# Optimization experiments

Hardware: AMD Instinct MI355X
Metric: run time of the kernel (lower is better)

The kernel has to match this reference:

```python
import jax, jax.numpy as jnp
import numpy as np

N_HEADS = 16
KQ_DIM = 64
EMB_DIM = 1024
CTX_DIM = 1024
EPS = 1e-5

def _layernorm(x, w, b):
    # LayerNorm over last dim (kq_dim), elementwise affine
    mu = jnp.mean(x, axis=-1, keepdims=True)
    var = jnp.mean(jnp.square(x - mu), axis=-1, keepdims=True)
    return (x - mu) * jax.lax.rsqrt(var + EPS) * w + b

def setup_inputs() -> dict:
    key = jax.random.key(0)
    ks = jax.random.split(key, 10)
    B, SQ, SK = 2, 2048, 2048
    inner = N_HEADS * KQ_DIM
    s_e = 1.0 / np.sqrt(EMB_DIM)
    s_c = 1.0 / np.sqrt(CTX_DIM)
    s_i = 1.0 / np.sqrt(inner)
    return {
        "emb": jax.random.normal(ks[0], (B, SQ, EMB_DIM), jnp.float32),
        "context": jax.random.normal(ks[1], (B, SK, CTX_DIM), jnp.float32),
        "Wq": jax.random.uniform(ks[2], (inner, EMB_DIM), jnp.float32, -s_e, s_e),
        "Wk": jax.random.uniform(ks[3], (inner, CTX_DIM), jnp.float32, -s_c, s_c),
        "Wv": jax.random.uniform(ks[4], (inner, CTX_DIM), jnp.float32, -s_c, s_c),
        "Wu": jax.random.uniform(ks[5], (EMB_DIM, inner), jnp.float32, -s_i, s_i),
        "bu": jax.random.uniform(ks[6], (EMB_DIM,), jnp.float32, -s_i, s_i),
        "qn_w": jnp.ones((KQ_DIM,), jnp.float32),
        "qn_b": jnp.zeros((KQ_DIM,), jnp.float32),
        "kn_w": jnp.ones((KQ_DIM,), jnp.float32),
        "kn_b": jnp.zeros((KQ_DIM,), jnp.float32),
    }

def reference(emb, context, Wq, Wk, Wv, Wu, bu, qn_w, qn_b, kn_w, kn_b):
    B, SQ, _ = emb.shape
    SK = context.shape[1]
    # projections (no bias), reshape to [B, H, S, D]
    q = (emb @ Wq.T).reshape(B, SQ, N_HEADS, KQ_DIM).transpose(0, 2, 1, 3)
    k = (context @ Wk.T).reshape(B, SK, N_HEADS, KQ_DIM).transpose(0, 2, 1, 3)
    v = (context @ Wv.T).reshape(B, SK, N_HEADS, KQ_DIM).transpose(0, 2, 1, 3)
    q = _layernorm(q, qn_w, qn_b)
    k = _layernorm(k, kn_w, kn_b)
    scale = 1.0 / jnp.sqrt(jnp.asarray(KQ_DIM, emb.dtype))
    attn = jnp.einsum('bhqd,bhkd->bhqk', q, k) * scale
    attn = jax.nn.softmax(attn, axis=-1)
    out = jnp.einsum('bhqk,bhkd->bhqd', attn, v)
    out = out.transpose(0, 2, 1, 3).reshape(B, SQ, N_HEADS * KQ_DIM)
    return out @ Wu.T + bu
```

## Files before the change

### kernel.cpp

```cpp
#include <hip/hip_runtime.h>


typedef __attribute__((ext_vector_type(8)))  short bf16x8;
typedef __attribute__((ext_vector_type(4)))  short bf16x4;
typedef __attribute__((ext_vector_type(4)))  float f32x4;
typedef __attribute__((ext_vector_type(16))) float f32x16;
typedef __attribute__((ext_vector_type(4)))  unsigned int u32x4;

typedef __attribute__((address_space(1))) const void cg_void;
typedef __attribute__((address_space(3))) void lds_void_t;

__device__ __forceinline__ void gl_lds16(const void* g, void* l){
  __builtin_amdgcn_global_load_lds((cg_void*)g, (lds_void_t*)l, 16, 0, 0);
}

__device__ __forceinline__ short f2b(float f){
  unsigned int u;
  __builtin_memcpy(&u, &f, 4);
  u += 0x7fffu + ((u >> 16) & 1u);
  return (short)(u >> 16);
}

__global__ __launch_bounds__(256) void cvt6_kernel(
    const float* __restrict__ emb, const float* __restrict__ ctx,
    const float* __restrict__ Wq, const float* __restrict__ Wk,
    const float* __restrict__ Wv, const float* __restrict__ Wu,
    short* __restrict__ o_emb, short* __restrict__ o_ctx,
    short* __restrict__ o_wq, short* __restrict__ o_wk,
    short* __restrict__ o_wv, short* __restrict__ o_wu)
{
  const long M1 = 1024L * 1024L, M4 = 4L * M1;
  long e = ((long)blockIdx.x * 256 + threadIdx.x) * 4;
  if (e >= 12L * M1) return;
  const float* src; short* dst; long off;
  if      (e <     M4)      { src = emb; dst = o_emb; off = e;           }
  else if (e < 2 * M4)      { src = ctx; dst = o_ctx; off = e - M4;      }
  else if (e < 2 * M4 + M1) { src = Wq;  dst = o_wq;  off = e - 2 * M4;  }
  else if (e < 2 * M4 + 2*M1){src = Wk;  dst = o_wk;  off = e - 2*M4 - M1;}
  else if (e < 2 * M4 + 3*M1){src = Wv;  dst = o_wv;  off = e - 2*M4 - 2*M1;}
  else                      { src = Wu;  dst = o_wu;  off = e - 2*M4 - 3*M1;}
  f32x4 v = *(const f32x4*)(src + off);
  bf16x4 o;
  o[0] = f2b(v[0]); o[1] = f2b(v[1]); o[2] = f2b(v[2]); o[3] = f2b(v[3]);
  *(bf16x4*)(dst + off) = o;
}

__global__ __launch_bounds__(256) void gemm_qkv_kernel(
    const short* __restrict__ embh, const short* __restrict__ ctxh,
    const short* __restrict__ Wqh, const short* __restrict__ Wkh,
    const short* __restrict__ Wvh,
    short* __restrict__ qo, short* __restrict__ ko, short* __restrict__ vto,
    const float* __restrict__ qw, const float* __restrict__ qb,
    const float* __restrict__ kw, const float* __restrict__ kb)
{
  const int K = 1024;
  __shared__ short As[128 * 64];
  __shared__ short Bs[128 * 64];
  const int tid  = threadIdx.x;
  const int wave = tid >> 6, lane = tid & 63;
  const int quad = lane >> 4, r16 = lane & 15;
  const int wm = (wave >> 1) * 64, wn = (wave & 1) * 64;

  const int task = blockIdx.y;
  int bn, bm, N;
  const short *A, *B;
  if (task == 2){
    bn = (blockIdx.x & 31) * 128; bm = (blockIdx.x >> 5) * 128; N = 4096;
    A = Wvh; B = ctxh;
  } else {
    bn = (blockIdx.x & 7) * 128; bm = (blockIdx.x >> 3) * 128; N = 1024;
    A = task ? ctxh : embh; B = task ? Wkh : Wqh;
  }

  f32x4 acc[4][4];
#pragma unroll
  for (int i = 0; i < 4; i++)
#pragma unroll
    for (int j = 0; j < 4; j++)
      acc[i][j] = (f32x4){0.f, 0.f, 0.f, 0.f};

  const size_t arow = (size_t)(bm + wave * 8 + (lane >> 3)) * K + (lane & 7) * 8;
  const size_t brow = (size_t)(bn + wave * 8 + (lane >> 3)) * K + (lane & 7) * 8;

  for (int k0 = 0; k0 < K; k0 += 64){
#pragma unroll
    for (int i = 0; i < 4; i++){
      gl_lds16(A + arow + (size_t)32 * i * K + k0, &As[wave * 512 + i * 2048]);
      gl_lds16(B + brow + (size_t)32 * i * K + k0, &Bs[wave * 512 + i * 2048]);
    }
    __syncthreads();
#pragma unroll
    for (int kk = 0; kk < 2; kk++){
      bf16x8 af[4], bq[4];
#pragma unroll
      for (int i = 0; i < 4; i++)
        af[i] = *(const bf16x8*)(&As[(wm + i*16 + r16) * 64 + kk*32 + quad*8]);
#pragma unroll
      for (int j = 0; j < 4; j++)
        bq[j] = *(const bf16x8*)(&Bs[(wn + j*16 + r16) * 64 + kk*32 + quad*8]);
#pragma unroll
      for (int i = 0; i < 4; i++)
#pragma unroll
        for (int j = 0; j < 4; j++)
          acc[i][j] = __builtin_amdgcn_mfma_f32_16x16x32_bf16(af[i], bq[j], acc[i][j], 0, 0, 0);
    }
    __syncthreads();
  }

  if (task < 2){
    short* Ch = task ? ko : qo;
    const float* lw = task ? kw : qw;
    const float* lb = task ? kb : qb;
    float wv[4], bv[4];
#pragma unroll
    for (int j = 0; j < 4; j++){ wv[j] = lw[j*16 + r16]; bv[j] = lb[j*16 + r16]; }
#pragma unroll
    for (int i = 0; i < 4; i++){
#pragma unroll
      for (int t = 0; t < 4; t++){
        float a[4];
#pragma unroll
        for (int j = 0; j < 4; j++) a[j] = acc[i][j][t];
        float s = a[0] + a[1] + a[2] + a[3];
        s += __shfl_xor(s, 1); s += __shfl_xor(s, 2);
        s += __shfl_xor(s, 4); s += __shfl_xor(s, 8);
        const float mu = s * 0.015625f;
        float d[4], sq = 0.f;
#pragma unroll
        for (int j = 0; j < 4; j++){ d[j] = a[j] - mu; sq += d[j]*d[j]; }
        sq += __shfl_xor(sq, 1); sq += __shfl_xor(sq, 2);
        sq += __shfl_xor(sq, 4); sq += __shfl_xor(sq, 8);
        const float si = rsqrtf(sq * 0.015625f + 1e-5f);
        const size_t row = (size_t)(bm + wm + i*16 + quad*4 + t);
#pragma unroll
        for (int j = 0; j < 4; j++)
          Ch[row * 1024 + (bn + wn + j*16 + r16)] = f2b(d[j] * si * wv[j] + bv[j]);
      }
    }
  } else {
#pragma unroll
    for (int i = 0; i < 4; i++){
#pragma unroll
      for (int j = 0; j < 4; j++){
        const int p = (r16 & 3) | ((j & 1) << 2) | (((r16 >> 2) & 1) << 3)
                      | (((r16 >> 3) & 1) << 4);
        const int col = ((bn + wn + j*16 + r16) & ~31) | p;
#pragma unroll
        for (int t = 0; t < 4; t++){
          const size_t row = (size_t)(bm + wm + i*16 + quad*4 + t);
          vto[row * (size_t)N + col] = f2b(acc[i][j][t]);
        }
      }
    }
  }
}

__global__ __launch_bounds__(256) void gemm_out_kernel(
    const short* __restrict__ A, const short* __restrict__ B,
    float* __restrict__ Cf, const float* __restrict__ bias)
{
  const int K = 1024, N = 1024;
  __shared__ short As[128 * 128];
  __shared__ short Bs[128 * 128];
  const int tid  = threadIdx.x;
  const int wave = tid >> 6, lane = tid & 63;
  const int quad = lane >> 4, r16 = lane & 15;
  const int wm = (wave >> 1) * 64, wn = (wave & 1) * 64;
  const int bm = blockIdx.y * 128, bn = blockIdx.x * 128;

  f32x4 acc[4][4];
#pragma unroll
  for (int i = 0; i < 4; i++)
#pragma unroll
    for (int j = 0; j < 4; j++)
      acc[i][j] = (f32x4){0.f, 0.f, 0.f, 0.f};

  const size_t arow = (size_t)(bm + wave * 4 + (lane >> 4)) * K + (lane & 15) * 8;
  const size_t brow = (size_t)(bn + wave * 4 + (lane >> 4)) * K + (lane & 15) * 8;

  for (int k0 = 0; k0 < K; k0 += 128){
#pragma unroll
    for (int i = 0; i < 8; i++){
      gl_lds16(A + arow + (size_t)16 * i * K + k0, &As[(wave * 4 + i * 16) * 128]);
      gl_lds16(B + brow + (size_t)16 * i * K + k0, &Bs[(wave * 4 + i * 16) * 128]);
    }
    __syncthreads();
#pragma unroll
    for (int kk = 0; kk < 4; kk++){
      bf16x8 af[4], bq[4];
#pragma unroll
      for (int i = 0; i < 4; i++)
        af[i] = *(const bf16x8*)(&As[(wm + i*16 + r16) * 128 + kk*32 + quad*8]);
#pragma unroll
      for (int j = 0; j < 4; j++)
        bq[j] = *(const bf16x8*)(&Bs[(wn + j*16 + r16) * 128 + kk*32 + quad*8]);
#pragma unroll
      for (int i = 0; i < 4; i++)
#pragma unroll
        for (int j = 0; j < 4; j++)
          acc[i][j] = __builtin_amdgcn_mfma_f32_16x16x32_bf16(af[i], bq[j], acc[i][j], 0, 0, 0);
    }
    __syncthreads();
  }

#pragma unroll
  for (int i = 0; i < 4; i++){
#pragma unroll
    for (int j = 0; j < 4; j++){
      const int col = bn + wn + j*16 + r16;
#pragma unroll
      for (int t = 0; t < 4; t++){
        const size_t row = (size_t)(bm + wm + i*16 + quad*4 + t);
        Cf[row * N + col] = acc[i][j][t] + bias[col];
      }
    }
  }
}

__global__ __launch_bounds__(512, 4) void flash2_kernel(
    const short* __restrict__ Q, const short* __restrict__ K,
    const short* __restrict__ Vt, short* __restrict__ O)
{
  __shared__ __align__(16) long long smem8[8192];
  short* Ks  = (short*)smem8;
  short* Vts = Ks + 16384;
  float* scr = (float*)smem8;

  const int tid = threadIdx.x;
  const int wave = tid >> 6, lane = tid & 63;
  const int half = wave >> 2, wg = wave & 3;
  const int hh = lane >> 5, q5 = lane & 31;
  const int qb = blockIdx.x, h = blockIdx.y, b = blockIdx.z;
  const int q0 = qb * 128 + wg * 32;

  const size_t kbase = ((size_t)b * 2048) * 1024 + (size_t)h * 64;
  const size_t vbase = ((size_t)h * 64) * 4096 + (size_t)b * 2048;

  bf16x8 qf[4];
  {
    const size_t qrow = ((size_t)b * 2048 + q0 + q5) * 1024 + (size_t)h * 64;
#pragma unroll
    for (int c = 0; c < 4; c++)
      qf[c] = *(const bf16x8*)(Q + qrow + c * 16 + hh * 8);
  }

  f32x16 oacc[2];
#pragma unroll
  for (int mt = 0; mt < 2; mt++)
#pragma unroll
    for (int t = 0; t < 16; t++) oacc[mt][t] = 0.f;
  float lsum = 0.f;

  const int srow = lane >> 3;
  const int csrc = ((lane & 7) ^ srow) * 8;
  const int wr0 = wg * 16;

#define STAGE(bufi, kt)                                                         \
  {                                                                             \
    const short* ks = K + kbase + (size_t)((kt) * 64 + wr0 + srow) * 1024 + csrc; \
    const short* vs = Vt + vbase + (size_t)(wr0 + srow) * 4096 + (kt) * 64 + csrc; \
    short* kd = Ks  + (half * 2 + (bufi)) * 4096 + wr0 * 64;                    \
    short* vd = Vts + (half * 2 + (bufi)) * 4096 + wr0 * 64;                    \
    gl_lds16(ks,            kd);                                                \
    gl_lds16(ks + 8 * 1024, kd + 512);                                          \
    gl_lds16(vs,            vd);                                                \
    gl_lds16(vs + 8 * 4096, vd + 512);                                          \
  }

  STAGE(0, half)

  for (int i = 0; i < 16; i++){
    const int buf = i & 1;
    __syncthreads();
    if (i + 1 < 16) STAGE(buf ^ 1, 2 * (i + 1) + half)

    const short* kb_l = Ks  + (half * 2 + buf) * 4096;
    const short* vb_l = Vts + (half * 2 + buf) * 4096;

#pragma unroll
    for (int s32 = 0; s32 < 2; s32++){
      f32x16 sacc;
#pragma unroll
      for (int t = 0; t < 16; t++) sacc[t] = 0.f;
      const int key = s32 * 32 + q5;
#pragma unroll
      for (int c = 0; c < 4; c++){
        bf16x8 kf = *(const bf16x8*)(&kb_l[key * 64 + (((2*c + hh) ^ (key & 7)) << 3)]);
        sacc = __builtin_amdgcn_mfma_f32_32x32x16_bf16(kf, qf[c], sacc, 0, 0, 0);
      }

      unsigned int pu[16];
#pragma unroll
      for (int t = 0; t < 16; t++){
        const float e = __builtin_amdgcn_exp2f(sacc[t] * 0.18033688f);
        lsum += e;
        unsigned int u; __builtin_memcpy(&u, &e, 4);
        pu[t] = u + 0x8000u;
      }

#pragma unroll
      for (int c = 0; c < 2; c++){
        u32x4 tmp;
        tmp[0] = __builtin_amdgcn_perm(pu[4*c + 1], pu[4*c + 0], 0x07060302u);
        tmp[1] = __builtin_amdgcn_perm(pu[4*c + 3], pu[4*c + 2], 0x07060302u);
        tmp[2] = __builtin_amdgcn_perm(pu[8 + 4*c + 1], pu[8 + 4*c + 0], 0x07060302u);
        tmp[3] = __builtin_amdgcn_perm(pu[8 + 4*c + 3], pu[8 + 4*c + 2], 0x07060302u);
        bf16x8 pf; __builtin_memcpy(&pf, &tmp, 16);
#pragma unroll
        for (int mt = 0; mt < 2; mt++){
          const int d = mt * 32 + q5;
          bf16x8 vf = *(const bf16x8*)(&vb_l[d * 64 + (((s32*4 + 2*c + hh) ^ (d & 7)) << 3)]);
          oacc[mt] = __builtin_amdgcn_mfma_f32_32x32x16_bf16(vf, pf, oacc[mt], 0, 0, 0);
        }
      }
    }
  }

  lsum += __shfl_xor(lsum, 32);
  __syncthreads();
  float* base = scr + (wg * 64 + lane) * 33;
  if (half == 1){
#pragma unroll
    for (int t = 0; t < 16; t++){ base[t] = oacc[0][t]; base[16 + t] = oacc[1][t]; }
    scr[8448 + wg * 64 + lane] = lsum;
  }
  __syncthreads();
  if (half == 0){
    const float l2 = scr[8448 + wg * 64 + lane];
    const float linv = 1.0f / (lsum + l2);
    const size_t orow = ((size_t)b * 2048 + q0 + q5) * 1024 + (size_t)h * 64;
#pragma unroll
    for (int mt = 0; mt < 2; mt++){
#pragma unroll
      for (int g = 0; g < 4; g++){
        bf16x4 o4;
#pragma unroll
        for (int u = 0; u < 4; u++)
          o4[u] = f2b((oacc[mt][g*4 + u] + base[mt*16 + g*4 + u]) * linv);
        *(bf16x4*)(O + orow + mt*32 + g*8 + 4*hh) = o4;
      }
    }
  }
}
#undef STAGE

extern "C" void kernel_launch(void* const* d_in, const int* in_sizes, int n_in,
                              void* d_out, int out_size, void* d_ws, size_t ws_size,
                              hipStream_t stream) {
  const float* emb  = (const float*)d_in[0];
  const float* ctx  = (const float*)d_in[1];
  const float* Wq   = (const float*)d_in[2];
  const float* Wk   = (const float*)d_in[3];
  const float* Wv   = (const float*)d_in[4];
  const float* Wu   = (const float*)d_in[5];
  const float* bu   = (const float*)d_in[6];
  const float* qn_w = (const float*)d_in[7];
  const float* qn_b = (const float*)d_in[8];
  const float* kn_w = (const float*)d_in[9];
  const float* kn_b = (const float*)d_in[10];
  float* out = (float*)d_out;

  const size_t BIG = (size_t)4096 * 1024;
  const size_t WSZ = (size_t)1024 * 1024;
  short* ws   = (short*)d_ws;
  short* embh = ws;
  short* ctxh = embh + BIG;
  short* Wqh  = ctxh + BIG;
  short* Wkh  = Wqh + WSZ;
  short* Wvh  = Wkh + WSZ;
  short* Wuh  = Wvh + WSZ;
  short* qh   = Wuh + WSZ;
  short* kh   = qh + BIG;
  short* vth  = kh + BIG;
  short* aoh  = vth + BIG;

  cvt6_kernel<<<12288, 256, 0, stream>>>(emb, ctx, Wq, Wk, Wv, Wu,
                                         embh, ctxh, Wqh, Wkh, Wvh, Wuh);

  gemm_qkv_kernel<<<dim3(256, 3), 256, 0, stream>>>(
      embh, ctxh, Wqh, Wkh, Wvh, qh, kh, vth,
      qn_w, qn_b, kn_w, kn_b);

  flash2_kernel<<<dim3(16, 16, 2), 512, 0, stream>>>(qh, kh, vth, aoh);

  gemm_out_kernel<<<dim3(8, 32), 256, 0, stream>>>(aoh, Wuh, out, bu);
}
```

Measured before the change: 231.9 us.

## Split-K gemm_out across two wave halves and reorder block indices

```diff
diff --git a/kernel.cpp b/kernel.cpp
--- a/kernel.cpp
+++ b/kernel.cpp
@@ -68,7 +68,7 @@
     bn = (blockIdx.x & 31) * 128; bm = (blockIdx.x >> 5) * 128; N = 4096;
     A = Wvh; B = ctxh;
   } else {
-    bn = (blockIdx.x & 7) * 128; bm = (blockIdx.x >> 3) * 128; N = 1024;
+    bm = (blockIdx.x & 31) * 128; bn = (blockIdx.x >> 5) * 128; N = 1024;
     A = task ? ctxh : embh; B = task ? Wkh : Wqh;
   }
 
@@ -155,18 +155,19 @@
   }
 }
 
-__global__ __launch_bounds__(256) void gemm_out_kernel(
+__global__ __launch_bounds__(512) void gemm_out_kernel(
     const short* __restrict__ A, const short* __restrict__ B,
     float* __restrict__ Cf, const float* __restrict__ bias)
 {
   const int K = 1024, N = 1024;
-  __shared__ short As[128 * 128];
-  __shared__ short Bs[128 * 128];
+  __shared__ short As[2][128 * 64];
+  __shared__ short Bs[2][128 * 64];
   const int tid  = threadIdx.x;
   const int wave = tid >> 6, lane = tid & 63;
+  const int half = wave >> 2, wg = wave & 3;
   const int quad = lane >> 4, r16 = lane & 15;
-  const int wm = (wave >> 1) * 64, wn = (wave & 1) * 64;
-  const int bm = blockIdx.y * 128, bn = blockIdx.x * 128;
+  const int wm = (wg >> 1) * 64, wn = (wg & 1) * 64;
+  const int bm = blockIdx.x * 128, bn = blockIdx.y * 128;
 
   f32x4 acc[4][4];
 #pragma unroll
@@ -175,25 +176,26 @@
     for (int j = 0; j < 4; j++)
       acc[i][j] = (f32x4){0.f, 0.f, 0.f, 0.f};
 
-  const size_t arow = (size_t)(bm + wave * 4 + (lane >> 4)) * K + (lane & 15) * 8;
-  const size_t brow = (size_t)(bn + wave * 4 + (lane >> 4)) * K + (lane & 15) * 8;
-
-  for (int k0 = 0; k0 < K; k0 += 128){
-#pragma unroll
-    for (int i = 0; i < 8; i++){
-      gl_lds16(A + arow + (size_t)16 * i * K + k0, &As[(wave * 4 + i * 16) * 128]);
-      gl_lds16(B + brow + (size_t)16 * i * K + k0, &Bs[(wave * 4 + i * 16) * 128]);
-    }
-    __syncthreads();
-#pragma unroll
-    for (int kk = 0; kk < 4; kk++){
+  const int kh = half * 512;
+  const size_t arow = (size_t)(bm + wg * 8 + (lane >> 3)) * K + kh + (lane & 7) * 8;
+  const size_t brow = (size_t)(bn + wg * 8 + (lane >> 3)) * K + kh + (lane & 7) * 8;
+
+  for (int k0 = 0; k0 < 512; k0 += 64){
+#pragma unroll
+    for (int i = 0; i < 4; i++){
+      gl_lds16(A + arow + (size_t)32 * i * K + k0, &As[half][wg * 512 + i * 2048]);
+      gl_lds16(B + brow + (size_t)32 * i * K + k0, &Bs[half][wg * 512 + i * 2048]);
+    }
+    __syncthreads();
+#pragma unroll
+    for (int kk = 0; kk < 2; kk++){
       bf16x8 af[4], bq[4];
 #pragma unroll
       for (int i = 0; i < 4; i++)
-        af[i] = *(const bf16x8*)(&As[(wm + i*16 + r16) * 128 + kk*32 + quad*8]);
+        af[i] = *(const bf16x8*)(&As[half][(wm + i*16 + r16) * 64 + kk*32 + quad*8]);
 #pragma unroll
       for (int j = 0; j < 4; j++)
-        bq[j] = *(const bf16x8*)(&Bs[(wn + j*16 + r16) * 128 + kk*32 + quad*8]);
+        bq[j] = *(const bf16x8*)(&Bs[half][(wn + j*16 + r16) * 64 + kk*32 + quad*8]);
 #pragma unroll
       for (int i = 0; i < 4; i++)
 #pragma unroll
@@ -203,17 +205,30 @@
     __syncthreads();
   }
 
+  float* scr = (float*)&As[0][0];
 #pragma unroll
   for (int i = 0; i < 4; i++){
-#pragma unroll
-    for (int j = 0; j < 4; j++){
-      const int col = bn + wn + j*16 + r16;
-#pragma unroll
-      for (int t = 0; t < 4; t++){
-        const size_t row = (size_t)(bm + wm + i*16 + quad*4 + t);
-        Cf[row * N + col] = acc[i][j][t] + bias[col];
-      }
-    }
+    if (half == 1){
+      float* p = scr + (wg * 64 + lane) * 17;
+#pragma unroll
+      for (int j = 0; j < 4; j++)
+#pragma unroll
+        for (int t = 0; t < 4; t++) p[j*4 + t] = acc[i][j][t];
+    }
+    __syncthreads();
+    if (half == 0){
+      const float* p = scr + (wg * 64 + lane) * 17;
+#pragma unroll
+      for (int j = 0; j < 4; j++){
+        const int col = bn + wn + j*16 + r16;
+#pragma unroll
+        for (int t = 0; t < 4; t++){
+          const size_t row = (size_t)(bm + wm + i*16 + quad*4 + t);
+          Cf[row * N + col] = acc[i][j][t] + p[j*4 + t] + bias[col];
+        }
+      }
+    }
+    __syncthreads();
   }
 }
 
@@ -230,7 +245,7 @@
   const int wave = tid >> 6, lane = tid & 63;
   const int half = wave >> 2, wg = wave & 3;
   const int hh = lane >> 5, q5 = lane & 31;
-  const int qb = blockIdx.x, h = blockIdx.y, b = blockIdx.z;
+  const int h = blockIdx.x, qb = blockIdx.y, b = blockIdx.z;
   const int q0 = qb * 128 + wg * 32;
 
   const size_t kbase = ((size_t)b * 2048) * 1024 + (size_t)h * 64;
@@ -383,5 +398,5 @@
 
   flash2_kernel<<<dim3(16, 16, 2), 512, 0, stream>>>(qh, kh, vth, aoh);
 
-  gemm_out_kernel<<<dim3(8, 32), 256, 0, stream>>>(aoh, Wuh, out, bu);
-}
+  gemm_out_kernel<<<dim3(32, 8), 512, 0, stream>>>(aoh, Wuh, out, bu);
+}
```

New measurement: 219.2 us. -5.4%, faster.
